# Kernel tuning notes

Hardware: AMD Instinct MI355X
Metric: run time of the kernel (lower is better)

## Reference

```python
import jax, jax.numpy as jnp
import numpy as np

B, S, H, NH = 2, 2048, 1024, 16
HD = H // NH  # head dim = 64


def setup_inputs() -> dict:
    key = jax.random.key(0)
    k_in, k_q, k_kv, k_o = jax.random.split(key, 4)
    scale = 0.02
    return {
        "inputs": jax.random.normal(k_in, (B, S, H), dtype=jnp.float32),
        "Wq": jax.random.normal(k_q, (H, H), dtype=jnp.float32) * scale,
        "bq": jnp.zeros((H,), dtype=jnp.float32),
        "Wkv": jax.random.normal(k_kv, (H, 2 * H), dtype=jnp.float32) * scale,
        "bkv": jnp.zeros((2 * H,), dtype=jnp.float32),
        "Wo": jax.random.normal(k_o, (H, H), dtype=jnp.float32) * scale,
        "bo": jnp.zeros((H,), dtype=jnp.float32),
    }


def reference(inputs, Wq, bq, Wkv, bkv, Wo, bo):
    b, s, h = inputs.shape
    q = inputs @ Wq + bq                      # [B,S,H]
    kv = inputs @ Wkv + bkv                   # [B,S,2H]
    k, v = kv[..., :h], kv[..., h:]           # each [B,S,H]
    q = q.reshape(b, s, NH, HD)
    k = k.reshape(b, s, NH, HD)
    v = v.reshape(b, s, NH, HD)
    inv_sqrt_d = jnp.asarray(1.0 / np.sqrt(HD), dtype=inputs.dtype)
    scores = jnp.einsum("bqhd,bkhd->bhqk", q, k) * inv_sqrt_d  # [B,NH,S,S]
    probs = jax.nn.softmax(scores, axis=-1)
    attended = jnp.einsum("bhqk,bkhd->bqhd", probs, v)         # [B,S,NH,HD]
    attended = attended.reshape(b, s, h)
    return attended @ Wo + bo
```

## Files before the change

kernel.cpp:

```cpp
#include <hip/hip_runtime.h>
#include <cstdint>

typedef __bf16 bf16;
typedef __attribute__((ext_vector_type(8))) __bf16 bf16x8;
typedef __attribute__((ext_vector_type(4))) __bf16 bf16v4;
typedef __attribute__((ext_vector_type(2))) __bf16 bf16x2;
typedef __attribute__((ext_vector_type(4))) float f32x4;
typedef __attribute__((ext_vector_type(16))) float f32x16;
typedef __attribute__((ext_vector_type(4))) unsigned u32x4;

#define MFMA16(a, b, c) __builtin_amdgcn_mfma_f32_16x16x32_bf16((a), (b), (c), 0, 0, 0)
#define MFMA32(a, b, c) __builtin_amdgcn_mfma_f32_32x32x16_bf16((a), (b), (c), 0, 0, 0)

#define BATCH 2
#define SLEN 2048
#define HDIM 1024
#define NHEAD 16
#define HEADD 64
#define MROWS (BATCH * SLEN)

#define CEXP 0.1803368801f

typedef __attribute__((address_space(3))) void lds_void;
typedef const __attribute__((address_space(1))) void glb_void;
__device__ __forceinline__ void load_lds16(const bf16* g, bf16* l) {
    __builtin_amdgcn_global_load_lds((glb_void*)g, (lds_void*)l, 16, 0, 0);
}

__device__ __forceinline__ void plswap(unsigned& a, unsigned& b) {
#if __has_builtin(__builtin_amdgcn_permlane32_swap)
    auto r = __builtin_amdgcn_permlane32_swap(a, b, false, false);
    a = r[0]; b = r[1];
#else
    asm volatile("v_permlane32_swap_b32 %0, %1" : "+v"(a), "+v"(b));
#endif
}

__global__ __launch_bounds__(256) void prep_kernel(const float* __restrict__ X,
                                                   const float* __restrict__ Wq,
                                                   const float* __restrict__ Wkv,
                                                   const float* __restrict__ Wo,
                                                   const float* __restrict__ bq,
                                                   const float* __restrict__ bkv,
                                                   bf16* __restrict__ Xbf,
                                                   bf16* __restrict__ WqkvT,
                                                   bf16* __restrict__ WoT,
                                                   float* __restrict__ bqkv) {
    const int blk = blockIdx.x;
    const int tid = threadIdx.x;
    if (blk < 4096) {
        int i = (blk * 256 + tid) * 4;
        float4 v = *(const float4*)&X[i];
        bf16v4 o;
        o[0] = (bf16)v.x; o[1] = (bf16)v.y; o[2] = (bf16)v.z; o[3] = (bf16)v.w;
        *(bf16v4*)&Xbf[i] = o;
        return;
    }
    if (blk < 8192) {
        const float* in; bf16* out; int C, id;
        if (blk < 5120)      { in = Wq;  out = WqkvT;                C = 1024; id = blk - 4096; }
        else if (blk < 7168) { in = Wkv; out = WqkvT + 1024 * 1024;  C = 2048; id = blk - 5120; }
        else                 { in = Wo;  out = WoT;                  C = 1024; id = blk - 7168; }
        const int R = 1024;
        const int nbx = C / 32;
        const int j0 = (id % nbx) * 32, i0 = (id / nbx) * 32;
        const int tx = tid & 31, ty = tid >> 5;
        __shared__ float t[32][33];
        for (int r = ty; r < 32; r += 8)
            t[r][tx] = in[(size_t)(i0 + r) * C + j0 + tx];
        __syncthreads();
        for (int r = ty; r < 32; r += 8)
            out[(size_t)(j0 + r) * R + i0 + tx] = (bf16)t[tx][r];
        return;
    }
    int i = (blk - 8192) * 256 + tid;
    if (i < 3072) bqkv[i] = (i < 1024) ? bq[i] : bkv[i - 1024];
}

template <int BM, int BN, int EPI>
__global__ __launch_bounds__(256) void gemm2_kernel(const bf16* __restrict__ A,
                                                    const bf16* __restrict__ BT,
                                                    const float* __restrict__ bias,
                                                    bf16* __restrict__ oQ,
                                                    bf16* __restrict__ oK,
                                                    bf16* __restrict__ oVT,
                                                    float* __restrict__ oF, int K) {
    constexpr int WM = BM / 2, WN = BN / 2;
    constexpr int MT = WM / 16, NT = WN / 16;

    const int tid = threadIdx.x;
    const int lane = tid & 63, wid = tid >> 6;
    const int l15 = lane & 15, quad = lane >> 4;
    const int wm = (wid >> 1) * WM, wn = (wid & 1) * WN;
    const int m0 = blockIdx.y * BM, n0 = blockIdx.x * BN;

    __shared__ bf16 As[BM * 32];
    __shared__ bf16 Bs[BN * 32];

    f32x4 acc[MT][NT] = {};

    const bf16* Ag = A + (size_t)m0 * K;
    const bf16* Bg = BT + (size_t)n0 * K;
    const int arow = lane >> 2, acol = (lane & 3) * 8;

    for (int k0 = 0; k0 < K; k0 += 32) {
#pragma unroll
        for (int t = 0; t < BM / 64; ++t) {
            int tt = t * 4 + wid;
            load_lds16(Ag + (size_t)(tt * 16 + arow) * K + k0 + acol, &As[tt * 512]);
        }
#pragma unroll
        for (int t = 0; t < BN / 64; ++t) {
            int tt = t * 4 + wid;
            load_lds16(Bg + (size_t)(tt * 16 + arow) * K + k0 + acol, &Bs[tt * 512]);
        }
        __syncthreads();

        bf16x8 af[MT], bfr[NT];
#pragma unroll
        for (int i = 0; i < MT; ++i)
            af[i] = *(const bf16x8*)&As[(wm + i * 16 + l15) * 32 + quad * 8];
#pragma unroll
        for (int j = 0; j < NT; ++j)
            bfr[j] = *(const bf16x8*)&Bs[(wn + j * 16 + l15) * 32 + quad * 8];
#pragma unroll
        for (int i = 0; i < MT; ++i)
#pragma unroll
            for (int j = 0; j < NT; ++j)
                acc[i][j] = MFMA16(af[i], bfr[j], acc[i][j]);
        __syncthreads();
    }

#pragma unroll
    for (int i = 0; i < MT; ++i) {
#pragma unroll
        for (int j = 0; j < NT; ++j) {
            const int mb = m0 + wm + i * 16 + quad * 4;
            const int n = n0 + wn + j * 16 + l15;
            const float bv = bias[n];
            if (EPI == 2) {
                float* o = oF + (size_t)mb * 1024 + n;
#pragma unroll
                for (int r = 0; r < 4; ++r) o[(size_t)r * 1024] = acc[i][j][r] + bv;
            } else if (n0 < 1024) {
#pragma unroll
                for (int r = 0; r < 4; ++r)
                    oQ[(size_t)(mb + r) * 1024 + n] = (bf16)((acc[i][j][r] + bv) * CEXP);
            } else if (n0 < 2048) {
#pragma unroll
                for (int r = 0; r < 4; ++r)
                    oK[(size_t)(mb + r) * 1024 + (n - 1024)] = (bf16)(acc[i][j][r] + bv);
            } else {
                const int hd = n - 2048;
                const int bb = mb >> 11, ss = mb & 2047;
                bf16v4 pk;
#pragma unroll
                for (int r = 0; r < 4; ++r) pk[r] = (bf16)(acc[i][j][r] + bv);
                *(bf16v4*)&oVT[((size_t)(bb << 10) + hd) * 2048 + ss] = pk;
            }
        }
    }
}

__global__ __launch_bounds__(256) void attn7_kernel(const bf16* __restrict__ Q,
                                                    const bf16* __restrict__ K,
                                                    const bf16* __restrict__ VT,
                                                    bf16* __restrict__ O) {
    const int bid = blockIdx.x;
    const int xcd = bid & 7, j = bid >> 3;
    const int bh = xcd * 4 + (j >> 4);
    const int q0 = (j & 15) * 128;
    const int b = bh >> 4, head = bh & 15;
    const int tid = threadIdx.x;
    const int lane = tid & 63, wid = tid >> 6;
    const int l31 = lane & 31, hh = lane >> 5;

    __shared__ bf16 Ks[2][128 * 64];
    __shared__ bf16 VTs[2][64 * 128];

    const int qw = q0 + wid * 32;
    bf16x8 qf[4];
#pragma unroll
    for (int kd = 0; kd < 4; ++kd)
        qf[kd] = *(const bf16x8*)&Q[(size_t)(b * SLEN + qw + l31) * HDIM +
                                    head * 64 + kd * 16 + hh * 8];

    f32x16 o_acc[2] = {};
    float l_lane = 0.f;

    const bf16* Kg = K + (size_t)b * SLEN * HDIM + head * 64;
    const bf16* Vg = VT + (size_t)bh * 64 * SLEN;

    const int r8 = lane >> 3, p8 = lane & 7;
    const int r16 = lane >> 4, p16 = lane & 15;

#pragma unroll
    for (int pass = 0; pass < 4; ++pass) {
        const int rbk = pass * 32 + wid * 8;
        load_lds16(Kg + (size_t)(rbk + r8) * HDIM + ((p8 ^ ((rbk + r8) & 7)) * 8),
                   &Ks[0][rbk * 64]);
        const int rbv = pass * 16 + wid * 4;
        load_lds16(Vg + (size_t)(rbv + r16) * SLEN + ((p16 ^ ((rbv + r16) & 15)) * 8),
                   &VTs[0][rbv * 128]);
    }

    for (int kt = 0; kt < 16; ++kt) {
        const int cur = kt & 1;
        if (kt < 15) {
            const int k0 = (kt + 1) * 128;
#pragma unroll
            for (int pass = 0; pass < 4; ++pass) {
                const int rbk = pass * 32 + wid * 8;
                load_lds16(Kg + (size_t)(k0 + rbk + r8) * HDIM + ((p8 ^ ((rbk + r8) & 7)) * 8),
                           &Ks[cur ^ 1][rbk * 64]);
                const int rbv = pass * 16 + wid * 4;
                load_lds16(Vg + (size_t)(rbv + r16) * SLEN + k0 + ((p16 ^ ((rbv + r16) & 15)) * 8),
                           &VTs[cur ^ 1][rbv * 128]);
            }
            asm volatile("s_waitcnt vmcnt(8)" ::: "memory");
        } else {
            asm volatile("s_waitcnt vmcnt(0)" ::: "memory");
        }
        __builtin_amdgcn_s_barrier();

        const bf16* Kc = &Ks[cur][0];
        const bf16* Vc = &VTs[cur][0];

#pragma unroll
        for (int h = 0; h < 2; ++h) {
            f32x16 sacc[2] = {};
#pragma unroll
            for (int kd = 0; kd < 4; ++kd)
#pragma unroll
                for (int m = 0; m < 2; ++m) {
                    const int key = (h * 2 + m) * 32 + l31;
                    const int c = (kd * 2 + hh) ^ (key & 7);
                    bf16x8 kf = *(const bf16x8*)&Kc[key * 64 + c * 8];
                    sacc[m] = MFMA32(kf, qf[kd], sacc[m]);
                }

            unsigned wA[2][4], wB[2][4];
#pragma unroll
            for (int m = 0; m < 2; ++m)
#pragma unroll
                for (int g = 0; g < 4; ++g) {
                    float p0 = __builtin_amdgcn_exp2f(sacc[m][g * 4 + 0]);
                    float p1 = __builtin_amdgcn_exp2f(sacc[m][g * 4 + 1]);
                    float p2 = __builtin_amdgcn_exp2f(sacc[m][g * 4 + 2]);
                    float p3 = __builtin_amdgcn_exp2f(sacc[m][g * 4 + 3]);
                    l_lane += (p0 + p1) + (p2 + p3);
                    bf16x2 a, c2;
                    a[0] = (bf16)p0; a[1] = (bf16)p1;
                    c2[0] = (bf16)p2; c2[1] = (bf16)p3;
                    wA[m][g] = __builtin_bit_cast(unsigned, a);
                    wB[m][g] = __builtin_bit_cast(unsigned, c2);
                }

#pragma unroll
            for (int s = 0; s < 4; ++s) {
                const int m = s >> 1, qa = (s & 1) * 2, qb = qa + 1;
                unsigned x0 = wA[m][qa], x2 = wA[m][qb];
                unsigned x1 = wB[m][qa], x3 = wB[m][qb];
                plswap(x0, x2);
                plswap(x1, x3);
                u32x4 fw;
                fw[0] = x0; fw[1] = x1; fw[2] = x2; fw[3] = x3;
                bf16x8 pf = __builtin_bit_cast(bf16x8, fw);
#pragma unroll
                for (int dt = 0; dt < 2; ++dt) {
                    const int d = dt * 32 + l31;
                    const int cc = ((h * 4 + s) * 2 + hh) ^ (d & 15);
                    bf16x8 vf = *(const bf16x8*)&Vc[d * 128 + cc * 8];
                    o_acc[dt] = MFMA32(vf, pf, o_acc[dt]);
                }
            }
        }
        asm volatile("" ::: "memory");
        __builtin_amdgcn_s_barrier();
    }

    const float l_full = l_lane + __shfl_xor(l_lane, 32, 64);
    const float inv = 1.f / l_full;
    bf16* orow = O + (size_t)(b * SLEN + qw + l31) * HDIM + head * 64;
#pragma unroll
    for (int mt = 0; mt < 2; ++mt)
#pragma unroll
        for (int g = 0; g < 4; ++g) {
            bf16v4 pk;
#pragma unroll
            for (int r = 0; r < 4; ++r) pk[r] = (bf16)(o_acc[mt][g * 4 + r] * inv);
            *(bf16v4*)&orow[mt * 32 + g * 8 + 4 * hh] = pk;
        }
}

extern "C" void kernel_launch(void* const* d_in, const int* in_sizes, int n_in,
                              void* d_out, int out_size, void* d_ws, size_t ws_size,
                              hipStream_t stream) {
    const float* X   = (const float*)d_in[0];
    const float* Wq  = (const float*)d_in[1];
    const float* bq  = (const float*)d_in[2];
    const float* Wkv = (const float*)d_in[3];
    const float* bkv = (const float*)d_in[4];
    const float* Wo  = (const float*)d_in[5];
    const float* bo  = (const float*)d_in[6];
    float* out = (float*)d_out;

    char* ws = (char*)d_ws;
    bf16* Xbf   = (bf16*)(ws);
    bf16* WqkvT = (bf16*)(ws + (8ull << 20));
    bf16* WoT   = (bf16*)(ws + (14ull << 20));
    float* bqkv = (float*)(ws + (16ull << 20));
    bf16* Qbf   = (bf16*)(ws + (17ull << 20));
    bf16* Kbf   = (bf16*)(ws + (25ull << 20));
    bf16* VTbf  = (bf16*)(ws + (33ull << 20));
    bf16* Abf   = (bf16*)(ws + (41ull << 20));

    prep_kernel<<<8204, 256, 0, stream>>>(X, Wq, Wkv, Wo, bq, bkv, Xbf, WqkvT, WoT, bqkv);

    gemm2_kernel<128, 128, 1><<<dim3(3072 / 128, MROWS / 128), 256, 0, stream>>>(
        Xbf, WqkvT, bqkv, Qbf, Kbf, VTbf, nullptr, 1024);

    attn7_kernel<<<512, 256, 0, stream>>>(Qbf, Kbf, VTbf, Abf);

    gemm2_kernel<128, 64, 2><<<dim3(1024 / 64, MROWS / 128), 256, 0, stream>>>(
        Abf, WoT, bo, nullptr, nullptr, nullptr, out, 1024);
}
```

Before: 196.6 us.

## Restructure attention inner loop with setprio, packed bf16 converts and staggered KV order

Result: no change. 194.3 us (-1.2%).

```diff
diff --git a/kernel.cpp b/kernel.cpp
--- a/kernel.cpp
+++ b/kernel.cpp
@@ -34,6 +34,12 @@
 #else
     asm volatile("v_permlane32_swap_b32 %0, %1" : "+v"(a), "+v"(b));
 #endif
+}
+
+__device__ __forceinline__ unsigned cvtpk_bf16(float lo, float hi) {
+    unsigned r;
+    asm("v_cvt_pk_bf16_f32 %0, %1, %2" : "=v"(r) : "v"(lo), "v"(hi));
+    return r;
 }
 
 __global__ __launch_bounds__(256) void prep_kernel(const float* __restrict__ X,
@@ -162,7 +168,37 @@
     }
 }
 
-__global__ __launch_bounds__(256) void attn7_kernel(const bf16* __restrict__ Q,
+__device__ __forceinline__ void sm_half(f32x16 sa, f32x16 sb, float& l_lane,
+                                        bf16x8* pf) {
+    unsigned wA[2][4], wB[2][4];
+#pragma unroll
+    for (int m = 0; m < 2; ++m) {
+        const f32x16 s = m ? sb : sa;
+#pragma unroll
+        for (int g = 0; g < 4; ++g) {
+            float p0 = __builtin_amdgcn_exp2f(s[g * 4 + 0]);
+            float p1 = __builtin_amdgcn_exp2f(s[g * 4 + 1]);
+            float p2 = __builtin_amdgcn_exp2f(s[g * 4 + 2]);
+            float p3 = __builtin_amdgcn_exp2f(s[g * 4 + 3]);
+            l_lane += (p0 + p1) + (p2 + p3);
+            wA[m][g] = cvtpk_bf16(p0, p1);
+            wB[m][g] = cvtpk_bf16(p2, p3);
+        }
+    }
+#pragma unroll
+    for (int s = 0; s < 4; ++s) {
+        const int m = s >> 1, qa = (s & 1) * 2, qb = qa + 1;
+        unsigned x0 = wA[m][qa], x2 = wA[m][qb];
+        unsigned x1 = wB[m][qa], x3 = wB[m][qb];
+        plswap(x0, x2);
+        plswap(x1, x3);
+        u32x4 fw;
+        fw[0] = x0; fw[1] = x1; fw[2] = x2; fw[3] = x3;
+        pf[s] = __builtin_bit_cast(bf16x8, fw);
+    }
+}
+
+__global__ __launch_bounds__(256) void attn8_kernel(const bf16* __restrict__ Q,
                                                     const bf16* __restrict__ K,
                                                     const bf16* __restrict__ VT,
                                                     bf16* __restrict__ O) {
@@ -186,6 +222,7 @@
                                     head * 64 + kd * 16 + hh * 8];
 
     f32x16 o_acc[2] = {};
+    const f32x16 ZC = {};
     float l_lane = 0.f;
 
     const bf16* Kg = K + (size_t)b * SLEN * HDIM + head * 64;
@@ -194,29 +231,28 @@
     const int r8 = lane >> 3, p8 = lane & 7;
     const int r16 = lane >> 4, p16 = lane & 15;
 
-#pragma unroll
-    for (int pass = 0; pass < 4; ++pass) {
-        const int rbk = pass * 32 + wid * 8;
-        load_lds16(Kg + (size_t)(rbk + r8) * HDIM + ((p8 ^ ((rbk + r8) & 7)) * 8),
-                   &Ks[0][rbk * 64]);
-        const int rbv = pass * 16 + wid * 4;
-        load_lds16(Vg + (size_t)(rbv + r16) * SLEN + ((p16 ^ ((rbv + r16) & 15)) * 8),
-                   &VTs[0][rbv * 128]);
-    }
+    const int ph = (j & 1) << 3;
+
+#define STAGE(buf, ktv) {                                                          \
+        const int k0_ = (((ktv) + ph) & 15) * 128;                                 \
+        _Pragma("unroll")                                                          \
+        for (int pass = 0; pass < 4; ++pass) {                                     \
+            const int rbk = pass * 32 + wid * 8;                                   \
+            load_lds16(Kg + (size_t)(k0_ + rbk + r8) * HDIM +                      \
+                           ((p8 ^ ((rbk + r8) & 7)) * 8),                          \
+                       &Ks[buf][rbk * 64]);                                        \
+            const int rbv = pass * 16 + wid * 4;                                   \
+            load_lds16(Vg + (size_t)(rbv + r16) * SLEN + k0_ +                     \
+                           ((p16 ^ ((rbv + r16) & 15)) * 8),                       \
+                       &VTs[buf][rbv * 128]);                                      \
+        } }
+
+    STAGE(0, 0)
 
     for (int kt = 0; kt < 16; ++kt) {
         const int cur = kt & 1;
         if (kt < 15) {
-            const int k0 = (kt + 1) * 128;
-#pragma unroll
-            for (int pass = 0; pass < 4; ++pass) {
-                const int rbk = pass * 32 + wid * 8;
-                load_lds16(Kg + (size_t)(k0 + rbk + r8) * HDIM + ((p8 ^ ((rbk + r8) & 7)) * 8),
-                           &Ks[cur ^ 1][rbk * 64]);
-                const int rbv = pass * 16 + wid * 4;
-                load_lds16(Vg + (size_t)(rbv + r16) * SLEN + k0 + ((p16 ^ ((rbv + r16) & 15)) * 8),
-                           &VTs[cur ^ 1][rbv * 128]);
-            }
+            STAGE(cur ^ 1, kt + 1)
             asm volatile("s_waitcnt vmcnt(8)" ::: "memory");
         } else {
             asm volatile("s_waitcnt vmcnt(0)" ::: "memory");
@@ -226,55 +262,55 @@
         const bf16* Kc = &Ks[cur][0];
         const bf16* Vc = &VTs[cur][0];
 
-#pragma unroll
-        for (int h = 0; h < 2; ++h) {
-            f32x16 sacc[2] = {};
-#pragma unroll
-            for (int kd = 0; kd < 4; ++kd)
-#pragma unroll
-                for (int m = 0; m < 2; ++m) {
-                    const int key = (h * 2 + m) * 32 + l31;
-                    const int c = (kd * 2 + hh) ^ (key & 7);
-                    bf16x8 kf = *(const bf16x8*)&Kc[key * 64 + c * 8];
-                    sacc[m] = MFMA32(kf, qf[kd], sacc[m]);
-                }
-
-            unsigned wA[2][4], wB[2][4];
-#pragma unroll
-            for (int m = 0; m < 2; ++m)
-#pragma unroll
-                for (int g = 0; g < 4; ++g) {
-                    float p0 = __builtin_amdgcn_exp2f(sacc[m][g * 4 + 0]);
-                    float p1 = __builtin_amdgcn_exp2f(sacc[m][g * 4 + 1]);
-                    float p2 = __builtin_amdgcn_exp2f(sacc[m][g * 4 + 2]);
-                    float p3 = __builtin_amdgcn_exp2f(sacc[m][g * 4 + 3]);
-                    l_lane += (p0 + p1) + (p2 + p3);
-                    bf16x2 a, c2;
-                    a[0] = (bf16)p0; a[1] = (bf16)p1;
-                    c2[0] = (bf16)p2; c2[1] = (bf16)p3;
-                    wA[m][g] = __builtin_bit_cast(unsigned, a);
-                    wB[m][g] = __builtin_bit_cast(unsigned, c2);
-                }
-
-#pragma unroll
-            for (int s = 0; s < 4; ++s) {
-                const int m = s >> 1, qa = (s & 1) * 2, qb = qa + 1;
-                unsigned x0 = wA[m][qa], x2 = wA[m][qb];
-                unsigned x1 = wB[m][qa], x3 = wB[m][qb];
-                plswap(x0, x2);
-                plswap(x1, x3);
-                u32x4 fw;
-                fw[0] = x0; fw[1] = x1; fw[2] = x2; fw[3] = x3;
-                bf16x8 pf = __builtin_bit_cast(bf16x8, fw);
-#pragma unroll
-                for (int dt = 0; dt < 2; ++dt) {
-                    const int d = dt * 32 + l31;
-                    const int cc = ((h * 4 + s) * 2 + hh) ^ (d & 15);
-                    bf16x8 vf = *(const bf16x8*)&Vc[d * 128 + cc * 8];
-                    o_acc[dt] = MFMA32(vf, pf, o_acc[dt]);
-                }
+        f32x16 s00, s01, s10, s11;
+        __builtin_amdgcn_s_setprio(1);
+#define QK_STEP(sv, h, m, kd, Cin) {                                       \
+        const int key_ = ((h) * 2 + (m)) * 32 + l31;                       \
+        const int c_ = ((kd) * 2 + hh) ^ (key_ & 7);                       \
+        bf16x8 kf_ = *(const bf16x8*)&Kc[key_ * 64 + c_ * 8];              \
+        sv = MFMA32(kf_, qf[kd], Cin); }
+        QK_STEP(s00, 0, 0, 0, ZC)
+        QK_STEP(s01, 0, 1, 0, ZC)
+        QK_STEP(s10, 1, 0, 0, ZC)
+        QK_STEP(s11, 1, 1, 0, ZC)
+#pragma unroll
+        for (int kd = 1; kd < 4; ++kd) {
+            QK_STEP(s00, 0, 0, kd, s00)
+            QK_STEP(s01, 0, 1, kd, s01)
+            QK_STEP(s10, 1, 0, kd, s10)
+            QK_STEP(s11, 1, 1, kd, s11)
+        }
+        __builtin_amdgcn_s_setprio(0);
+
+        bf16x8 pf0[4], pf1[4];
+        sm_half(s00, s01, l_lane, pf0);
+
+        __builtin_amdgcn_s_setprio(1);
+#pragma unroll
+        for (int s = 0; s < 4; ++s)
+#pragma unroll
+            for (int dt = 0; dt < 2; ++dt) {
+                const int d = dt * 32 + l31;
+                const int cc = (s * 2 + hh) ^ (d & 15);
+                bf16x8 vf = *(const bf16x8*)&Vc[d * 128 + cc * 8];
+                o_acc[dt] = MFMA32(vf, pf0[s], o_acc[dt]);
             }
-        }
+        __builtin_amdgcn_s_setprio(0);
+
+        sm_half(s10, s11, l_lane, pf1);
+
+        __builtin_amdgcn_s_setprio(1);
+#pragma unroll
+        for (int s = 0; s < 4; ++s)
+#pragma unroll
+            for (int dt = 0; dt < 2; ++dt) {
+                const int d = dt * 32 + l31;
+                const int cc = ((4 + s) * 2 + hh) ^ (d & 15);
+                bf16x8 vf = *(const bf16x8*)&Vc[d * 128 + cc * 8];
+                o_acc[dt] = MFMA32(vf, pf1[s], o_acc[dt]);
+            }
+        __builtin_amdgcn_s_setprio(0);
+
         asm volatile("" ::: "memory");
         __builtin_amdgcn_s_barrier();
     }
@@ -320,7 +356,7 @@
     gemm2_kernel<128, 128, 1><<<dim3(3072 / 128, MROWS / 128), 256, 0, stream>>>(
         Xbf, WqkvT, bqkv, Qbf, Kbf, VTbf, nullptr, 1024);
 
-    attn7_kernel<<<512, 256, 0, stream>>>(Qbf, Kbf, VTbf, Abf);
+    attn8_kernel<<<512, 256, 0, stream>>>(Qbf, Kbf, VTbf, Abf);
 
     gemm2_kernel<128, 64, 2><<<dim3(1024 / 64, MROWS / 128), 256, 0, stream>>>(
         Abf, WoT, bo, nullptr, nullptr, nullptr, out, 1024);
```
